# Kernel optimization log

Hardware: AMD Instinct MI355X
Metric: run time of the kernel (lower is better)

## Reference

```python
import jax, jax.numpy as jnp
import numpy as np

N, C, E = 32768, 256, 16
LN_EPS = 1e-5
ENT_EPS = 1e-12


def setup_inputs() -> dict:
    key = jax.random.key(0)
    ks = jax.random.split(key, 8)
    return {
        "inputs": jax.random.normal(ks[0], (N, C), jnp.float32),
        "conv_out": jax.random.normal(ks[1], (N, C), jnp.float32),
        "domain_emb": jax.random.normal(ks[2], (C,), jnp.float32),
        "share_W": jax.random.normal(ks[3], (C, C), jnp.float32) * 0.02,
        "share_b": jnp.zeros((C,), jnp.float32),
        "gate_W": jax.random.normal(ks[4], (C, E), jnp.float32) * 0.1,
        "gate_b": jnp.zeros((E,), jnp.float32),
        "expert_W": jax.random.normal(ks[5], (E, C, C), jnp.float32) * 0.02,
        "expert_b": jnp.zeros((E, C), jnp.float32),
        "ln_gamma": jnp.ones((C,), jnp.float32),
        "ln_beta": jnp.zeros((C,), jnp.float32),
    }


def reference(inputs, conv_out, domain_emb, share_W, share_b, gate_W, gate_b,
              expert_W, expert_b, ln_gamma, ln_beta):
    n_exp = gate_W.shape[-1]

    # shared expert
    share_out = inputs @ share_W + share_b                      # (N, C)

    # LayerNorm on (stand-in) sparse-conv features + domain embedding
    mu = conv_out.mean(-1, keepdims=True)
    var = conv_out.var(-1, keepdims=True)
    route = (conv_out - mu) / jnp.sqrt(var + LN_EPS) * ln_gamma + ln_beta
    route = route + domain_emb                                   # (N, C)

    # router (eval path: no noise)
    gate_logits = route @ gate_W + gate_b                        # (N, E)
    w = jax.nn.softmax(gate_logits.astype(jnp.float32), axis=-1).astype(inputs.dtype)

    # entropy -> dynamic k per token
    entropy = -jnp.sum(w * jnp.log(w + ENT_EPS), axis=-1)        # (N,)
    max_entropy = jnp.log(jnp.float32(n_exp))
    k = jnp.ceil(1.0 + entropy / max_entropy * (n_exp - 1)).astype(jnp.int32)
    k = jnp.clip(k, 1, n_exp)                                    # (N,)

    # dynamic top-k selection mask (sort descending, keep first k)
    order = jnp.argsort(-w, axis=-1)                             # (N, E) descending ranks
    positions = jnp.arange(n_exp)[None, :]
    mask_sorted = positions < k[:, None]                         # (N, E) bool
    inv = jnp.argsort(order, axis=-1)                            # inverse permutation
    sel_mask = jnp.take_along_axis(mask_sorted, inv, axis=-1)    # (N, E) bool, expert-order
    combine = jnp.where(sel_mask, w, jnp.zeros_like(w))          # (N, E) combine weights

    # Switch-style load balancing loss
    frac_tokens = sel_mask.astype(jnp.float32).mean(0)           # (E,)
    frac_probs = w.astype(jnp.float32).mean(0)                   # (E,)
    loss_balance = jnp.mean(frac_tokens * frac_probs) * (n_exp ** 2)

    # expert compute + combine (dense, equivalent to gather/scatter loop)
    expert_out = jnp.einsum('nc,ecd->ned', inputs, expert_W) + expert_b  # (N, E, C)
    moe_out = jnp.einsum('ne,nec->nc', combine, expert_out)     # (N, C)

    return moe_out + share_out, loss_balance
```

## Files before the change

kernel.cpp:

```cpp
#include <hip/hip_runtime.h>
#include <hip/hip_bf16.h>

#define NTOK 32768
#define CH   256
#define NEXP 16

typedef __attribute__((ext_vector_type(8)))  short short8;
typedef __attribute__((ext_vector_type(16))) float f32x16;

#define MFMA32(a, b, c) __builtin_amdgcn_mfma_f32_32x32x16_bf16((a), (b), (c), 0, 0, 0)
#define BC8(v) __builtin_bit_cast(short8, (v))

#define GLD16(lds, g) __builtin_amdgcn_global_load_lds(                          \
    (const __attribute__((address_space(1))) unsigned int*)(g),                  \
    (__attribute__((address_space(3))) unsigned int*)(lds), 16, 0, 0)

static __device__ __forceinline__ unsigned short f2bf(float f) {
  unsigned int u = __builtin_bit_cast(unsigned int, f);
  unsigned int r = (u + 0x7fffu + ((u >> 16) & 1u)) >> 16;
  return (unsigned short)r;
}


__global__ __launch_bounds__(256) void wconvert_kernel(
    const float* __restrict__ share_W, const float* __restrict__ expert_W,
    uint4* __restrict__ wp) {
  int g = blockIdx.x * 256 + threadIdx.x;
  int e = g >> 13;
  int r = g & 8191;
  int lane = r & 63;
  int kb = (r >> 6) & 15;
  int db = r >> 10;
  int d  = db * 32 + (lane & 31);
  int k0 = kb * 16 + ((lane >> 5) << 3);
  const float* src = (e < 16) ? (expert_W + (size_t)e * 65536) : share_W;
  unsigned int p[4];
#pragma unroll
  for (int j = 0; j < 4; j++) {
    float f0 = src[(size_t)(k0 + 2 * j) * 256 + d];
    float f1 = src[(size_t)(k0 + 2 * j + 1) * 256 + d];
    p[j] = (unsigned int)f2bf(f0) | ((unsigned int)f2bf(f1) << 16);
  }
  wp[g] = make_uint4(p[0], p[1], p[2], p[3]);
}

__global__ __launch_bounds__(512, 2) void gate_kernel(
    const float* __restrict__ inputs, const float* __restrict__ conv_out,
    const float* __restrict__ domain_emb, const float* __restrict__ gate_W,
    const float* __restrict__ gate_b, const float* __restrict__ ln_gamma,
    const float* __restrict__ ln_beta, uint4* __restrict__ apack,
    float* __restrict__ combine, float* __restrict__ frac_part) {
  __shared__ __align__(16) unsigned short atile[64 * 256];
  __shared__ __align__(16) float gwT[16 * 260];
  __shared__ float route[8][256];
  __shared__ float fred[2][8][16];
  int t = threadIdx.x, b = blockIdx.x;
  int w = t >> 6, l = t & 63;

  for (int i = 0; i < 8; i++) {
    int idx = i * 512 + t;
    gwT[(idx & 15) * 260 + (idx >> 4)] = gate_W[idx];
  }

  for (int i = 0; i < 4; i++) {
    int idx = i * 512 + t;
    int row = idx >> 5;
    int j = idx & 31;
    const float4* src = (const float4*)(inputs + ((size_t)b * 64 + row) * 256 + j * 8);
    float4 f0 = src[0], f1 = src[1];
    unsigned int p0 = (unsigned int)f2bf(f0.x) | ((unsigned int)f2bf(f0.y) << 16);
    unsigned int p1 = (unsigned int)f2bf(f0.z) | ((unsigned int)f2bf(f0.w) << 16);
    unsigned int p2 = (unsigned int)f2bf(f1.x) | ((unsigned int)f2bf(f1.y) << 16);
    unsigned int p3 = (unsigned int)f2bf(f1.z) | ((unsigned int)f2bf(f1.w) << 16);
    int s = j ^ (row & 31);
    *(uint4*)(atile + (row * 32 + s) * 8) = make_uint4(p0, p1, p2, p3);
  }
  __syncthreads();
  for (int i = 0; i < 4; i++) {
    int L = i * 512 + t;
    int ll = L & 63;
    int mb = (L >> 6) & 1, kb = L >> 7;
    int row = mb * 32 + (ll & 31);
    int j = kb * 2 + (ll >> 5);
    int s = j ^ (row & 31);
    apack[(size_t)b * 2048 + L] = *(const uint4*)(atile + (row * 32 + s) * 8);
  }

  int lc = l * 4;
  float4 g4 = *(const float4*)(ln_gamma + lc);
  float4 be4 = *(const float4*)(ln_beta + lc);
  float4 de4 = *(const float4*)(domain_emb + lc);
  int e = l & 15, q = l >> 4;
  float gb = gate_b[e];
  float psel = 0.f, pw = 0.f;

  float4 gwreg[16];
#pragma unroll
  for (int ii = 0; ii < 16; ii++)
    gwreg[ii] = *(const float4*)&gwT[e * 260 + q * 64 + ii * 4];

  int n0 = b * 64 + w * 8;
  float4 x = *(const float4*)(conv_out + (size_t)n0 * 256 + lc);
  for (int i = 0; i < 8; i++) {
    float4 xn = *(const float4*)(conv_out + (size_t)(n0 + ((i + 1) & 7)) * 256 + lc);

    float s1 = x.x + x.y + x.z + x.w;
#pragma unroll
    for (int off = 1; off < 64; off <<= 1) s1 += __shfl_xor(s1, off);
    float mu = s1 * (1.f / 256.f);
    float dx = x.x - mu, dy = x.y - mu, dz = x.z - mu, dw = x.w - mu;
    float s2 = dx * dx + dy * dy + dz * dz + dw * dw;
#pragma unroll
    for (int off = 1; off < 64; off <<= 1) s2 += __shfl_xor(s2, off);
    float rstd = rsqrtf(s2 * (1.f / 256.f) + 1e-5f);
    float4 r;
    r.x = dx * rstd * g4.x + be4.x + de4.x;
    r.y = dy * rstd * g4.y + be4.y + de4.y;
    r.z = dz * rstd * g4.z + be4.z + de4.z;
    r.w = dw * rstd * g4.w + be4.w + de4.w;
    *(float4*)(&route[w][lc]) = r;
    asm volatile("s_waitcnt lgkmcnt(0)" ::: "memory");
    __builtin_amdgcn_wave_barrier();

    float a0 = 0.f, a1 = 0.f, a2 = 0.f, a3 = 0.f;
#pragma unroll
    for (int ii = 0; ii < 16; ii += 4) {
      float4 r0 = *(const float4*)(&route[w][q * 64 + (ii + 0) * 4]);
      float4 r1 = *(const float4*)(&route[w][q * 64 + (ii + 1) * 4]);
      float4 r2 = *(const float4*)(&route[w][q * 64 + (ii + 2) * 4]);
      float4 r3 = *(const float4*)(&route[w][q * 64 + (ii + 3) * 4]);
      a0 += r0.x * gwreg[ii + 0].x + r0.y * gwreg[ii + 0].y + r0.z * gwreg[ii + 0].z + r0.w * gwreg[ii + 0].w;
      a1 += r1.x * gwreg[ii + 1].x + r1.y * gwreg[ii + 1].y + r1.z * gwreg[ii + 1].z + r1.w * gwreg[ii + 1].w;
      a2 += r2.x * gwreg[ii + 2].x + r2.y * gwreg[ii + 2].y + r2.z * gwreg[ii + 2].z + r2.w * gwreg[ii + 2].w;
      a3 += r3.x * gwreg[ii + 3].x + r3.y * gwreg[ii + 3].y + r3.z * gwreg[ii + 3].z + r3.w * gwreg[ii + 3].w;
    }
    float acc = (a0 + a1) + (a2 + a3);
    acc += __shfl_xor(acc, 16);
    acc += __shfl_xor(acc, 32);
    float logit = acc + gb;

    float m = logit;
#pragma unroll
    for (int off = 1; off < 16; off <<= 1) m = fmaxf(m, __shfl_xor(m, off));
    float p = expf(logit - m);
    float sum = p;
#pragma unroll
    for (int off = 1; off < 16; off <<= 1) sum += __shfl_xor(sum, off);
    float wv = p / sum;

    float et = -wv * logf(wv + 1e-12f);
    float ent = et;
#pragma unroll
    for (int off = 1; off < 16; off <<= 1) ent += __shfl_xor(ent, off);
    float kf = ceilf(1.f + ent * (15.f / 2.7725887f));
    int k = (int)kf;
    k = max(1, min(16, k));

    int base = l & 48;
    int rank = 0;
#pragma unroll
    for (int j = 0; j < 16; j++) {
      float wj = __shfl(wv, base + j);
      rank += (wj > wv) || (wj == wv && j < e);
    }
    int sel = rank < k;
    float cmb = sel ? wv : 0.f;
    int n = n0 + i;
    if (l < 16) combine[(size_t)n * 16 + e] = cmb;
    psel += (float)sel;
    pw += wv;

    x = xn;
  }

  if (l < 16) { fred[0][w][l] = psel; fred[1][w][l] = pw; }
  __syncthreads();
  if (t < 32) {
    int kind = t >> 4, ee = t & 15;
    float v = 0.f;
#pragma unroll
    for (int ww = 0; ww < 8; ww++) v += fred[kind][ww][ee];
    frac_part[b * 32 + t] = v;
  }
}

static __device__ __forceinline__ void pref_b(
    uint4 (&breg)[8], const uint4* __restrict__ we, int q) {
#pragma unroll
  for (int f = 0; f < 8; f++) {
    int kbl = f >> 1, d = f & 1;
    breg[f] = we[(size_t)d * 1024 + (q * 4 + kbl) * 64];
  }
}

static __device__ __forceinline__ void slot_mfma(
    f32x16 (&tacc)[2][2], const f32x16& zc, const uint4* __restrict__ ab,
    const uint4 (&breg)[8], int q, bool first) {
  __builtin_amdgcn_s_setprio(1);
#pragma unroll
  for (int kbl = 0; kbl < 4; kbl++) {
    short8 a0 = BC8(ab[(q * 4 + kbl) * 256]);
    short8 a1 = BC8(ab[(q * 4 + kbl) * 256 + 64]);
    short8 b0 = BC8(breg[kbl * 2 + 0]);
    short8 b1 = BC8(breg[kbl * 2 + 1]);
    if (first && kbl == 0) {
      tacc[0][0] = MFMA32(a0, b0, zc);
      tacc[0][1] = MFMA32(a0, b1, zc);
      tacc[1][0] = MFMA32(a1, b0, zc);
      tacc[1][1] = MFMA32(a1, b1, zc);
    } else {
      tacc[0][0] = MFMA32(a0, b0, tacc[0][0]);
      tacc[0][1] = MFMA32(a0, b1, tacc[0][1]);
      tacc[1][0] = MFMA32(a1, b0, tacc[1][0]);
      tacc[1][1] = MFMA32(a1, b1, tacc[1][1]);
    }
  }
  __builtin_amdgcn_s_setprio(0);
}

__global__ __launch_bounds__(512, 2) void moe_gemm_kernel(
    const uint4* __restrict__ apack, const uint4* __restrict__ wpack,
    const float* __restrict__ combine, const float* __restrict__ expert_b,
    const float* __restrict__ share_b, float* __restrict__ out) {
  extern __shared__ __align__(16) char smem[];
  uint4* atile = (uint4*)smem;
  float* wtile = (float*)(smem + 65536);

  int t = threadIdx.x, b = blockIdx.x;
  int w = t >> 6, l = t & 63;
  int mbp = w >> 2;
  int dbp = w & 3;

#pragma unroll
  for (int i = 0; i < 8; i++) {
    int g = w * 8 + i;
    int kb = g >> 2, mb = g & 3;
    const uint4* src = apack + ((size_t)(2 * b + (mb >> 1)) * 2048 + (size_t)(kb * 2 + (mb & 1)) * 64 + l);
    GLD16(atile + g * 64, src);
  }
  {
    const float* cg = combine + (size_t)b * 2048;
#pragma unroll
    for (int i = 0; i < 4; i++) {
      int idx = i * 512 + t;
      wtile[(idx & 15) * 128 + (idx >> 4)] = cg[idx];
    }
  }
  __syncthreads();

  f32x16 facc[2][2];
#pragma unroll
  for (int mi = 0; mi < 2; mi++)
#pragma unroll
    for (int d = 0; d < 2; d++)
#pragma unroll
      for (int r = 0; r < 16; r++) facc[mi][d][r] = 0.f;
  f32x16 zc;
#pragma unroll
  for (int r = 0; r < 16; r++) zc[r] = 0.f;

  f32x16 tacc[2][2];
  int rowoff = (l >> 5) * 4;

  const uint4* ab = atile + (size_t)(mbp * 2) * 64 + l;
  const uint4* wb = wpack + (size_t)(dbp * 2) * 1024 + l;

  uint4 bregA[8], bregB[8];
  pref_b(bregA, wb, 0);

  for (int e = 0; e < 17; e++) {
    const uint4* we = wb + (size_t)e * 8192;
    pref_b(bregB, we, 1);
    slot_mfma(tacc, zc, ab, bregA, 0, true);
    pref_b(bregA, we, 2);
    slot_mfma(tacc, zc, ab, bregB, 1, false);
    pref_b(bregB, we, 3);
    slot_mfma(tacc, zc, ab, bregA, 2, false);
    if (e < 16) pref_b(bregA, we + 8192, 0);
    slot_mfma(tacc, zc, ab, bregB, 3, false);

    if (e < 16) {
#pragma unroll
      for (int mi = 0; mi < 2; mi++)
#pragma unroll
        for (int rg = 0; rg < 4; rg++) {
          float4 w4 = *(const float4*)&wtile[e * 128 + (mbp * 2 + mi) * 32 + 8 * rg + rowoff];
          float wj[4] = {w4.x, w4.y, w4.z, w4.w};
#pragma unroll
          for (int j = 0; j < 4; j++) {
            facc[mi][0][rg * 4 + j] += wj[j] * tacc[mi][0][rg * 4 + j];
            facc[mi][1][rg * 4 + j] += wj[j] * tacc[mi][1][rg * 4 + j];
          }
        }
    } else {
#pragma unroll
      for (int mi = 0; mi < 2; mi++)
#pragma unroll
        for (int r = 0; r < 16; r++) {
          facc[mi][0][r] += tacc[mi][0][r];
          facc[mi][1][r] += tacc[mi][1][r];
        }
    }
  }

  int col = l & 31;
  int cg0 = (dbp * 2 + 0) * 32 + col;
  int cg1 = (dbp * 2 + 1) * 32 + col;
  float sb0 = share_b[cg0], sb1 = share_b[cg1];
  float eb0[16], eb1[16];
#pragma unroll
  for (int e2 = 0; e2 < 16; e2++) {
    eb0[e2] = expert_b[e2 * 256 + cg0];
    eb1[e2] = expert_b[e2 * 256 + cg1];
  }
#pragma unroll
  for (int e2 = 0; e2 < 16; e2++)
#pragma unroll
    for (int mi = 0; mi < 2; mi++)
#pragma unroll
      for (int rg = 0; rg < 4; rg++) {
        float4 w4 = *(const float4*)&wtile[e2 * 128 + (mbp * 2 + mi) * 32 + 8 * rg + rowoff];
        float wj[4] = {w4.x, w4.y, w4.z, w4.w};
#pragma unroll
        for (int j = 0; j < 4; j++) {
          facc[mi][0][rg * 4 + j] += wj[j] * eb0[e2];
          facc[mi][1][rg * 4 + j] += wj[j] * eb1[e2];
        }
      }
#pragma unroll
  for (int mi = 0; mi < 2; mi++)
#pragma unroll
    for (int r = 0; r < 16; r++) {
      int row = (mbp * 2 + mi) * 32 + (r & 3) + ((r >> 2) << 3) + rowoff;
      size_t n = (size_t)b * 128 + row;
      out[n * 256 + cg0] = facc[mi][0][r] + sb0;
      out[n * 256 + cg1] = facc[mi][1][r] + sb1;
    }
}

__global__ __launch_bounds__(256) void finalize_kernel(
    const float* __restrict__ frac_part, float* __restrict__ loss_out) {
  __shared__ float acc[8][32];
  int t = threadIdx.x;
  int col = t & 31, seg = t >> 5;
  float s = 0.f;
  for (int i = seg; i < 512; i += 8) s += frac_part[i * 32 + col];
  acc[seg][col] = s;
  __syncthreads();
  if (t < 32) {
    float v = 0.f;
#pragma unroll
    for (int sg = 0; sg < 8; sg++) v += acc[sg][t];
    acc[0][t] = v;
  }
  __syncthreads();
  if (t == 0) {
    float loss = 0.f;
    for (int e = 0; e < 16; e++) {
      float ft = acc[0][e] * (1.f / 32768.f);
      float fp = acc[0][16 + e] * (1.f / 32768.f);
      loss += ft * fp;
    }
    loss_out[0] = loss * 16.f;
  }
}

extern "C" void kernel_launch(void* const* d_in, const int* in_sizes, int n_in,
                              void* d_out, int out_size, void* d_ws, size_t ws_size,
                              hipStream_t stream) {
  const float* inputs   = (const float*)d_in[0];
  const float* conv_out = (const float*)d_in[1];
  const float* demb     = (const float*)d_in[2];
  const float* share_W  = (const float*)d_in[3];
  const float* share_b  = (const float*)d_in[4];
  const float* gate_W   = (const float*)d_in[5];
  const float* gate_b   = (const float*)d_in[6];
  const float* expert_W = (const float*)d_in[7];
  const float* expert_b = (const float*)d_in[8];
  const float* ln_g     = (const float*)d_in[9];
  const float* ln_b     = (const float*)d_in[10];
  float* out = (float*)d_out;
  char* ws = (char*)d_ws;

  uint4* apack   = (uint4*)(ws);
  uint4* wpack   = (uint4*)(ws + 16777216);
  float* combine = (float*)(ws + 19005440);
  float* frac    = (float*)(ws + 21102592);

  hipFuncSetAttribute((const void*)moe_gemm_kernel,
                      hipFuncAttributeMaxDynamicSharedMemorySize, 73728);

  wconvert_kernel<<<dim3(544), dim3(256), 0, stream>>>(share_W, expert_W, wpack);
  gate_kernel<<<dim3(512), dim3(512), 0, stream>>>(inputs, conv_out, demb, gate_W,
                                                   gate_b, ln_g, ln_b, apack, combine, frac);
  moe_gemm_kernel<<<dim3(256), dim3(512), 73728, stream>>>(apack, wpack, combine,
                                                           expert_b, share_b, out);
  finalize_kernel<<<dim3(1), dim3(256), 0, stream>>>(frac, out + 8388608);
}
```

Before: 241.0 us.

## Fuse gating and expert GEMM into one kernel, removing apack/combine round trips

Merges the gate kernel (LayerNorm, router, softmax, entropy-based top-k) with the MoE GEMM kernel so the bf16 input tile and the combine weights stay in LDS instead of going through global workspace. The gate weight transpose moves into an extra block of the weight-convert kernel. The GEMM tile shrinks to 64 rows per block with one 32-column block per wave, and occupancy rises to 4 blocks. Each block now re-streams all expert weights for half as many rows, which doubles weight traffic from L2, and MFMA reuse per weight load drops.

```diff
diff --git a/kernel.cpp b/kernel.cpp
--- a/kernel.cpp
+++ b/kernel.cpp
@@ -10,10 +10,6 @@
 
 #define MFMA32(a, b, c) __builtin_amdgcn_mfma_f32_32x32x16_bf16((a), (b), (c), 0, 0, 0)
 #define BC8(v) __builtin_bit_cast(short8, (v))
-
-#define GLD16(lds, g) __builtin_amdgcn_global_load_lds(                          \
-    (const __attribute__((address_space(1))) unsigned int*)(g),                  \
-    (__attribute__((address_space(3))) unsigned int*)(lds), 16, 0, 0)
 
 static __device__ __forceinline__ unsigned short f2bf(float f) {
   unsigned int u = __builtin_bit_cast(unsigned int, f);
@@ -24,7 +20,17 @@
 
 __global__ __launch_bounds__(256) void wconvert_kernel(
     const float* __restrict__ share_W, const float* __restrict__ expert_W,
-    uint4* __restrict__ wp) {
+    const float* __restrict__ gate_W, uint4* __restrict__ wp,
+    float* __restrict__ gwt) {
+  if (blockIdx.x == 544) {
+    int t = threadIdx.x;
+#pragma unroll
+    for (int i = 0; i < 16; i++) {
+      int idx = i * 256 + t;
+      gwt[(idx & 15) * 256 + (idx >> 4)] = gate_W[idx];
+    }
+    return;
+  }
   int g = blockIdx.x * 256 + threadIdx.x;
   int e = g >> 13;
   int r = g & 8191;
@@ -44,297 +50,232 @@
   wp[g] = make_uint4(p[0], p[1], p[2], p[3]);
 }
 
-__global__ __launch_bounds__(512, 2) void gate_kernel(
+static __device__ __forceinline__ void slot_mfma4(
+    f32x16 (&tacc)[2], const f32x16& zc, const uint4* __restrict__ at,
+    const uint4 (&breg)[4], int q, int r5, int hi, bool first) {
+  __builtin_amdgcn_s_setprio(1);
+#pragma unroll
+  for (int kbl = 0; kbl < 4; kbl++) {
+    int kb = q * 4 + kbl;
+    int ai = r5 * 32 + ((kb * 2 + hi) ^ r5);
+    short8 a0 = BC8(at[ai]);
+    short8 a1 = BC8(at[1024 + ai]);
+    short8 bb = BC8(breg[kbl]);
+    if (first && kbl == 0) {
+      tacc[0] = MFMA32(a0, bb, zc);
+      tacc[1] = MFMA32(a1, bb, zc);
+    } else {
+      tacc[0] = MFMA32(a0, bb, tacc[0]);
+      tacc[1] = MFMA32(a1, bb, tacc[1]);
+    }
+  }
+  __builtin_amdgcn_s_setprio(0);
+}
+
+__global__ __launch_bounds__(512, 4) void moe_fused_kernel(
     const float* __restrict__ inputs, const float* __restrict__ conv_out,
-    const float* __restrict__ domain_emb, const float* __restrict__ gate_W,
+    const float* __restrict__ domain_emb, const float* __restrict__ gwt,
     const float* __restrict__ gate_b, const float* __restrict__ ln_gamma,
-    const float* __restrict__ ln_beta, uint4* __restrict__ apack,
-    float* __restrict__ combine, float* __restrict__ frac_part) {
-  __shared__ __align__(16) unsigned short atile[64 * 256];
-  __shared__ __align__(16) float gwT[16 * 260];
-  __shared__ float route[8][256];
-  __shared__ float fred[2][8][16];
+    const float* __restrict__ ln_beta, const uint4* __restrict__ wpack,
+    const float* __restrict__ expert_b, const float* __restrict__ share_b,
+    float* __restrict__ out, float* __restrict__ frac_part) {
+  extern __shared__ __align__(16) char smem[];
+  uint4* at    = (uint4*)smem;
+  float* wtile = (float*)(smem + 32768);
+  float* route = (float*)(smem + 36864);
+
   int t = threadIdx.x, b = blockIdx.x;
   int w = t >> 6, l = t & 63;
-
-  for (int i = 0; i < 8; i++) {
-    int idx = i * 512 + t;
-    gwT[(idx & 15) * 260 + (idx >> 4)] = gate_W[idx];
-  }
-
+  int dbp = w;
+  int r5 = l & 31, hi = l >> 5;
+
+#pragma unroll
   for (int i = 0; i < 4; i++) {
     int idx = i * 512 + t;
-    int row = idx >> 5;
-    int j = idx & 31;
-    const float4* src = (const float4*)(inputs + ((size_t)b * 64 + row) * 256 + j * 8);
+    int r = idx >> 5, j = idx & 31;
+    const float4* src = (const float4*)(inputs + ((size_t)b * 64 + r) * 256 + j * 8);
     float4 f0 = src[0], f1 = src[1];
     unsigned int p0 = (unsigned int)f2bf(f0.x) | ((unsigned int)f2bf(f0.y) << 16);
     unsigned int p1 = (unsigned int)f2bf(f0.z) | ((unsigned int)f2bf(f0.w) << 16);
     unsigned int p2 = (unsigned int)f2bf(f1.x) | ((unsigned int)f2bf(f1.y) << 16);
     unsigned int p3 = (unsigned int)f2bf(f1.z) | ((unsigned int)f2bf(f1.w) << 16);
-    int s = j ^ (row & 31);
-    *(uint4*)(atile + (row * 32 + s) * 8) = make_uint4(p0, p1, p2, p3);
-  }
-  __syncthreads();
-  for (int i = 0; i < 4; i++) {
-    int L = i * 512 + t;
-    int ll = L & 63;
-    int mb = (L >> 6) & 1, kb = L >> 7;
-    int row = mb * 32 + (ll & 31);
-    int j = kb * 2 + (ll >> 5);
-    int s = j ^ (row & 31);
-    apack[(size_t)b * 2048 + L] = *(const uint4*)(atile + (row * 32 + s) * 8);
-  }
-
-  int lc = l * 4;
-  float4 g4 = *(const float4*)(ln_gamma + lc);
-  float4 be4 = *(const float4*)(ln_beta + lc);
-  float4 de4 = *(const float4*)(domain_emb + lc);
-  int e = l & 15, q = l >> 4;
-  float gb = gate_b[e];
-  float psel = 0.f, pw = 0.f;
-
-  float4 gwreg[16];
-#pragma unroll
-  for (int ii = 0; ii < 16; ii++)
-    gwreg[ii] = *(const float4*)&gwT[e * 260 + q * 64 + ii * 4];
-
-  int n0 = b * 64 + w * 8;
-  float4 x = *(const float4*)(conv_out + (size_t)n0 * 256 + lc);
-  for (int i = 0; i < 8; i++) {
-    float4 xn = *(const float4*)(conv_out + (size_t)(n0 + ((i + 1) & 7)) * 256 + lc);
-
-    float s1 = x.x + x.y + x.z + x.w;
-#pragma unroll
-    for (int off = 1; off < 64; off <<= 1) s1 += __shfl_xor(s1, off);
-    float mu = s1 * (1.f / 256.f);
-    float dx = x.x - mu, dy = x.y - mu, dz = x.z - mu, dw = x.w - mu;
-    float s2 = dx * dx + dy * dy + dz * dz + dw * dw;
-#pragma unroll
-    for (int off = 1; off < 64; off <<= 1) s2 += __shfl_xor(s2, off);
-    float rstd = rsqrtf(s2 * (1.f / 256.f) + 1e-5f);
-    float4 r;
-    r.x = dx * rstd * g4.x + be4.x + de4.x;
-    r.y = dy * rstd * g4.y + be4.y + de4.y;
-    r.z = dz * rstd * g4.z + be4.z + de4.z;
-    r.w = dw * rstd * g4.w + be4.w + de4.w;
-    *(float4*)(&route[w][lc]) = r;
-    asm volatile("s_waitcnt lgkmcnt(0)" ::: "memory");
-    __builtin_amdgcn_wave_barrier();
-
-    float a0 = 0.f, a1 = 0.f, a2 = 0.f, a3 = 0.f;
-#pragma unroll
-    for (int ii = 0; ii < 16; ii += 4) {
-      float4 r0 = *(const float4*)(&route[w][q * 64 + (ii + 0) * 4]);
-      float4 r1 = *(const float4*)(&route[w][q * 64 + (ii + 1) * 4]);
-      float4 r2 = *(const float4*)(&route[w][q * 64 + (ii + 2) * 4]);
-      float4 r3 = *(const float4*)(&route[w][q * 64 + (ii + 3) * 4]);
-      a0 += r0.x * gwreg[ii + 0].x + r0.y * gwreg[ii + 0].y + r0.z * gwreg[ii + 0].z + r0.w * gwreg[ii + 0].w;
-      a1 += r1.x * gwreg[ii + 1].x + r1.y * gwreg[ii + 1].y + r1.z * gwreg[ii + 1].z + r1.w * gwreg[ii + 1].w;
-      a2 += r2.x * gwreg[ii + 2].x + r2.y * gwreg[ii + 2].y + r2.z * gwreg[ii + 2].z + r2.w * gwreg[ii + 2].w;
-      a3 += r3.x * gwreg[ii + 3].x + r3.y * gwreg[ii + 3].y + r3.z * gwreg[ii + 3].z + r3.w * gwreg[ii + 3].w;
-    }
-    float acc = (a0 + a1) + (a2 + a3);
-    acc += __shfl_xor(acc, 16);
-    acc += __shfl_xor(acc, 32);
-    float logit = acc + gb;
-
-    float m = logit;
-#pragma unroll
-    for (int off = 1; off < 16; off <<= 1) m = fmaxf(m, __shfl_xor(m, off));
-    float p = expf(logit - m);
-    float sum = p;
-#pragma unroll
-    for (int off = 1; off < 16; off <<= 1) sum += __shfl_xor(sum, off);
-    float wv = p / sum;
-
-    float et = -wv * logf(wv + 1e-12f);
-    float ent = et;
-#pragma unroll
-    for (int off = 1; off < 16; off <<= 1) ent += __shfl_xor(ent, off);
-    float kf = ceilf(1.f + ent * (15.f / 2.7725887f));
-    int k = (int)kf;
-    k = max(1, min(16, k));
-
-    int base = l & 48;
-    int rank = 0;
-#pragma unroll
-    for (int j = 0; j < 16; j++) {
-      float wj = __shfl(wv, base + j);
-      rank += (wj > wv) || (wj == wv && j < e);
-    }
-    int sel = rank < k;
-    float cmb = sel ? wv : 0.f;
-    int n = n0 + i;
-    if (l < 16) combine[(size_t)n * 16 + e] = cmb;
-    psel += (float)sel;
-    pw += wv;
-
-    x = xn;
-  }
-
-  if (l < 16) { fred[0][w][l] = psel; fred[1][w][l] = pw; }
-  __syncthreads();
-  if (t < 32) {
-    int kind = t >> 4, ee = t & 15;
-    float v = 0.f;
-#pragma unroll
-    for (int ww = 0; ww < 8; ww++) v += fred[kind][ww][ee];
-    frac_part[b * 32 + t] = v;
-  }
-}
-
-static __device__ __forceinline__ void pref_b(
-    uint4 (&breg)[8], const uint4* __restrict__ we, int q) {
-#pragma unroll
-  for (int f = 0; f < 8; f++) {
-    int kbl = f >> 1, d = f & 1;
-    breg[f] = we[(size_t)d * 1024 + (q * 4 + kbl) * 64];
-  }
-}
-
-static __device__ __forceinline__ void slot_mfma(
-    f32x16 (&tacc)[2][2], const f32x16& zc, const uint4* __restrict__ ab,
-    const uint4 (&breg)[8], int q, bool first) {
-  __builtin_amdgcn_s_setprio(1);
-#pragma unroll
-  for (int kbl = 0; kbl < 4; kbl++) {
-    short8 a0 = BC8(ab[(q * 4 + kbl) * 256]);
-    short8 a1 = BC8(ab[(q * 4 + kbl) * 256 + 64]);
-    short8 b0 = BC8(breg[kbl * 2 + 0]);
-    short8 b1 = BC8(breg[kbl * 2 + 1]);
-    if (first && kbl == 0) {
-      tacc[0][0] = MFMA32(a0, b0, zc);
-      tacc[0][1] = MFMA32(a0, b1, zc);
-      tacc[1][0] = MFMA32(a1, b0, zc);
-      tacc[1][1] = MFMA32(a1, b1, zc);
-    } else {
-      tacc[0][0] = MFMA32(a0, b0, tacc[0][0]);
-      tacc[0][1] = MFMA32(a0, b1, tacc[0][1]);
-      tacc[1][0] = MFMA32(a1, b0, tacc[1][0]);
-      tacc[1][1] = MFMA32(a1, b1, tacc[1][1]);
-    }
-  }
-  __builtin_amdgcn_s_setprio(0);
-}
-
-__global__ __launch_bounds__(512, 2) void moe_gemm_kernel(
-    const uint4* __restrict__ apack, const uint4* __restrict__ wpack,
-    const float* __restrict__ combine, const float* __restrict__ expert_b,
-    const float* __restrict__ share_b, float* __restrict__ out) {
-  extern __shared__ __align__(16) char smem[];
-  uint4* atile = (uint4*)smem;
-  float* wtile = (float*)(smem + 65536);
-
-  int t = threadIdx.x, b = blockIdx.x;
-  int w = t >> 6, l = t & 63;
-  int mbp = w >> 2;
-  int dbp = w & 3;
-
-#pragma unroll
-  for (int i = 0; i < 8; i++) {
-    int g = w * 8 + i;
-    int kb = g >> 2, mb = g & 3;
-    const uint4* src = apack + ((size_t)(2 * b + (mb >> 1)) * 2048 + (size_t)(kb * 2 + (mb & 1)) * 64 + l);
-    GLD16(atile + g * 64, src);
-  }
+    at[r * 32 + (j ^ (r & 31))] = make_uint4(p0, p1, p2, p3);
+  }
+
+  const uint4* wb = wpack + (size_t)dbp * 1024 + l;
+  uint4 bregA[4], bregB[4];
+#pragma unroll
+  for (int kbl = 0; kbl < 4; kbl++) bregA[kbl] = wb[kbl * 64];
+
   {
-    const float* cg = combine + (size_t)b * 2048;
-#pragma unroll
-    for (int i = 0; i < 4; i++) {
-      int idx = i * 512 + t;
-      wtile[(idx & 15) * 128 + (idx >> 4)] = cg[idx];
-    }
-  }
-  __syncthreads();
-
-  f32x16 facc[2][2];
+    int lc = l * 4;
+    float4 g4 = *(const float4*)(ln_gamma + lc);
+    float4 be4 = *(const float4*)(ln_beta + lc);
+    float4 de4 = *(const float4*)(domain_emb + lc);
+    int e = l & 15, q = l >> 4;
+    float gb = gate_b[e];
+    const float4* gv4 = (const float4*)(gwt + e * 256 + q * 64);
+    float psel = 0.f, pw = 0.f;
+
+    int n0 = b * 64 + w * 8;
+    float4 x = *(const float4*)(conv_out + (size_t)n0 * 256 + lc);
+    for (int i = 0; i < 8; i++) {
+      float4 xn = *(const float4*)(conv_out + (size_t)(n0 + ((i + 1) & 7)) * 256 + lc);
+
+      float s1 = x.x + x.y + x.z + x.w;
+#pragma unroll
+      for (int off = 1; off < 64; off <<= 1) s1 += __shfl_xor(s1, off);
+      float mu = s1 * (1.f / 256.f);
+      float dx = x.x - mu, dy = x.y - mu, dz = x.z - mu, dw = x.w - mu;
+      float s2 = dx * dx + dy * dy + dz * dz + dw * dw;
+#pragma unroll
+      for (int off = 1; off < 64; off <<= 1) s2 += __shfl_xor(s2, off);
+      float rstd = rsqrtf(s2 * (1.f / 256.f) + 1e-5f);
+      float4 r;
+      r.x = dx * rstd * g4.x + be4.x + de4.x;
+      r.y = dy * rstd * g4.y + be4.y + de4.y;
+      r.z = dz * rstd * g4.z + be4.z + de4.z;
+      r.w = dw * rstd * g4.w + be4.w + de4.w;
+      *(float4*)(&route[w * 256 + lc]) = r;
+      asm volatile("s_waitcnt lgkmcnt(0)" ::: "memory");
+      __builtin_amdgcn_wave_barrier();
+
+      float a0 = 0.f, a1 = 0.f, a2 = 0.f, a3 = 0.f;
+#pragma unroll
+      for (int ii = 0; ii < 16; ii += 4) {
+        float4 r0 = *(const float4*)(&route[w * 256 + q * 64 + (ii + 0) * 4]);
+        float4 r1 = *(const float4*)(&route[w * 256 + q * 64 + (ii + 1) * 4]);
+        float4 r2 = *(const float4*)(&route[w * 256 + q * 64 + (ii + 2) * 4]);
+        float4 r3 = *(const float4*)(&route[w * 256 + q * 64 + (ii + 3) * 4]);
+        float4 g0 = gv4[ii + 0], g1 = gv4[ii + 1], g2 = gv4[ii + 2], g3 = gv4[ii + 3];
+        a0 += r0.x * g0.x + r0.y * g0.y + r0.z * g0.z + r0.w * g0.w;
+        a1 += r1.x * g1.x + r1.y * g1.y + r1.z * g1.z + r1.w * g1.w;
+        a2 += r2.x * g2.x + r2.y * g2.y + r2.z * g2.z + r2.w * g2.w;
+        a3 += r3.x * g3.x + r3.y * g3.y + r3.z * g3.z + r3.w * g3.w;
+      }
+      float acc = (a0 + a1) + (a2 + a3);
+      acc += __shfl_xor(acc, 16);
+      acc += __shfl_xor(acc, 32);
+      float logit = acc + gb;
+
+      float m = logit;
+#pragma unroll
+      for (int off = 1; off < 16; off <<= 1) m = fmaxf(m, __shfl_xor(m, off));
+      float p = expf(logit - m);
+      float sum = p;
+#pragma unroll
+      for (int off = 1; off < 16; off <<= 1) sum += __shfl_xor(sum, off);
+      float wv = p / sum;
+
+      float et = -wv * logf(wv + 1e-12f);
+      float ent = et;
+#pragma unroll
+      for (int off = 1; off < 16; off <<= 1) ent += __shfl_xor(ent, off);
+      float kf = ceilf(1.f + ent * (15.f / 2.7725887f));
+      int k = (int)kf;
+      k = max(1, min(16, k));
+
+      int base = l & 48;
+      int rank = 0;
+#pragma unroll
+      for (int j = 0; j < 16; j++) {
+        float wj = __shfl(wv, base + j);
+        rank += (wj > wv) || (wj == wv && j < e);
+      }
+      int sel = rank < k;
+      float cmb = sel ? wv : 0.f;
+      if (l < 16) wtile[e * 64 + (w * 8 + i)] = cmb;
+      psel += (float)sel;
+      pw += wv;
+
+      x = xn;
+    }
+
+    __syncthreads();
+    if (l < 16) {
+      route[0 * 128 + w * 16 + l] = psel;
+      route[1 * 128 + w * 16 + l] = pw;
+    }
+    __syncthreads();
+    if (t < 32) {
+      int kind = t >> 4, ee = t & 15;
+      float v = 0.f;
+#pragma unroll
+      for (int ww = 0; ww < 8; ww++) v += route[kind * 128 + ww * 16 + ee];
+      frac_part[b * 32 + t] = v;
+    }
+  }
+
+  f32x16 facc[2];
 #pragma unroll
   for (int mi = 0; mi < 2; mi++)
 #pragma unroll
-    for (int d = 0; d < 2; d++)
-#pragma unroll
-      for (int r = 0; r < 16; r++) facc[mi][d][r] = 0.f;
+    for (int r = 0; r < 16; r++) facc[mi][r] = 0.f;
   f32x16 zc;
 #pragma unroll
   for (int r = 0; r < 16; r++) zc[r] = 0.f;
-
-  f32x16 tacc[2][2];
-  int rowoff = (l >> 5) * 4;
-
-  const uint4* ab = atile + (size_t)(mbp * 2) * 64 + l;
-  const uint4* wb = wpack + (size_t)(dbp * 2) * 1024 + l;
-
-  uint4 bregA[8], bregB[8];
-  pref_b(bregA, wb, 0);
+  f32x16 tacc[2];
+  int rowoff = hi * 4;
 
   for (int e = 0; e < 17; e++) {
     const uint4* we = wb + (size_t)e * 8192;
-    pref_b(bregB, we, 1);
-    slot_mfma(tacc, zc, ab, bregA, 0, true);
-    pref_b(bregA, we, 2);
-    slot_mfma(tacc, zc, ab, bregB, 1, false);
-    pref_b(bregB, we, 3);
-    slot_mfma(tacc, zc, ab, bregA, 2, false);
-    if (e < 16) pref_b(bregA, we + 8192, 0);
-    slot_mfma(tacc, zc, ab, bregB, 3, false);
-
+#pragma unroll
+    for (int kbl = 0; kbl < 4; kbl++) bregB[kbl] = we[(4 + kbl) * 64];
+    slot_mfma4(tacc, zc, at, bregA, 0, r5, hi, true);
+#pragma unroll
+    for (int kbl = 0; kbl < 4; kbl++) bregA[kbl] = we[(8 + kbl) * 64];
+    slot_mfma4(tacc, zc, at, bregB, 1, r5, hi, false);
+#pragma unroll
+    for (int kbl = 0; kbl < 4; kbl++) bregB[kbl] = we[(12 + kbl) * 64];
+    slot_mfma4(tacc, zc, at, bregA, 2, r5, hi, false);
     if (e < 16) {
 #pragma unroll
+      for (int kbl = 0; kbl < 4; kbl++) bregA[kbl] = we[8192 + kbl * 64];
+    }
+    slot_mfma4(tacc, zc, at, bregB, 3, r5, hi, false);
+
+    if (e < 16) {
+#pragma unroll
       for (int mi = 0; mi < 2; mi++)
 #pragma unroll
         for (int rg = 0; rg < 4; rg++) {
-          float4 w4 = *(const float4*)&wtile[e * 128 + (mbp * 2 + mi) * 32 + 8 * rg + rowoff];
+          float4 w4 = *(const float4*)&wtile[e * 64 + mi * 32 + 8 * rg + rowoff];
           float wj[4] = {w4.x, w4.y, w4.z, w4.w};
 #pragma unroll
-          for (int j = 0; j < 4; j++) {
-            facc[mi][0][rg * 4 + j] += wj[j] * tacc[mi][0][rg * 4 + j];
-            facc[mi][1][rg * 4 + j] += wj[j] * tacc[mi][1][rg * 4 + j];
-          }
+          for (int j = 0; j < 4; j++)
+            facc[mi][rg * 4 + j] += wj[j] * tacc[mi][rg * 4 + j];
         }
     } else {
 #pragma unroll
       for (int mi = 0; mi < 2; mi++)
 #pragma unroll
-        for (int r = 0; r < 16; r++) {
-          facc[mi][0][r] += tacc[mi][0][r];
-          facc[mi][1][r] += tacc[mi][1][r];
-        }
-    }
-  }
-
-  int col = l & 31;
-  int cg0 = (dbp * 2 + 0) * 32 + col;
-  int cg1 = (dbp * 2 + 1) * 32 + col;
-  float sb0 = share_b[cg0], sb1 = share_b[cg1];
-  float eb0[16], eb1[16];
-#pragma unroll
-  for (int e2 = 0; e2 < 16; e2++) {
-    eb0[e2] = expert_b[e2 * 256 + cg0];
-    eb1[e2] = expert_b[e2 * 256 + cg1];
-  }
+        for (int r = 0; r < 16; r++) facc[mi][r] += tacc[mi][r];
+    }
+  }
+
+  int col = dbp * 32 + r5;
+  float sb = share_b[col];
+  float eb[16];
+#pragma unroll
+  for (int e2 = 0; e2 < 16; e2++) eb[e2] = expert_b[e2 * 256 + col];
 #pragma unroll
   for (int e2 = 0; e2 < 16; e2++)
 #pragma unroll
     for (int mi = 0; mi < 2; mi++)
 #pragma unroll
       for (int rg = 0; rg < 4; rg++) {
-        float4 w4 = *(const float4*)&wtile[e2 * 128 + (mbp * 2 + mi) * 32 + 8 * rg + rowoff];
+        float4 w4 = *(const float4*)&wtile[e2 * 64 + mi * 32 + 8 * rg + rowoff];
         float wj[4] = {w4.x, w4.y, w4.z, w4.w};
 #pragma unroll
-        for (int j = 0; j < 4; j++) {
-          facc[mi][0][rg * 4 + j] += wj[j] * eb0[e2];
-          facc[mi][1][rg * 4 + j] += wj[j] * eb1[e2];
-        }
+        for (int j = 0; j < 4; j++)
+          facc[mi][rg * 4 + j] += wj[j] * eb[e2];
       }
 #pragma unroll
   for (int mi = 0; mi < 2; mi++)
 #pragma unroll
     for (int r = 0; r < 16; r++) {
-      int row = (mbp * 2 + mi) * 32 + (r & 3) + ((r >> 2) << 3) + rowoff;
-      size_t n = (size_t)b * 128 + row;
-      out[n * 256 + cg0] = facc[mi][0][r] + sb0;
-      out[n * 256 + cg1] = facc[mi][1][r] + sb1;
+      int row = mi * 32 + (r & 3) + ((r >> 2) << 3) + rowoff;
+      out[((size_t)b * 64 + row) * 256 + col] = facc[mi][r] + sb;
     }
 }
 
@@ -382,18 +323,17 @@
   float* out = (float*)d_out;
   char* ws = (char*)d_ws;
 
-  uint4* apack   = (uint4*)(ws);
-  uint4* wpack   = (uint4*)(ws + 16777216);
-  float* combine = (float*)(ws + 19005440);
-  float* frac    = (float*)(ws + 21102592);
-
-  hipFuncSetAttribute((const void*)moe_gemm_kernel,
-                      hipFuncAttributeMaxDynamicSharedMemorySize, 73728);
-
-  wconvert_kernel<<<dim3(544), dim3(256), 0, stream>>>(share_W, expert_W, wpack);
-  gate_kernel<<<dim3(512), dim3(512), 0, stream>>>(inputs, conv_out, demb, gate_W,
-                                                   gate_b, ln_g, ln_b, apack, combine, frac);
-  moe_gemm_kernel<<<dim3(256), dim3(512), 73728, stream>>>(apack, wpack, combine,
-                                                           expert_b, share_b, out);
+  uint4* wpack = (uint4*)(ws);
+  float* gwt   = (float*)(ws + 2228224);
+  float* frac  = (float*)(ws + 2244608);
+
+  hipFuncSetAttribute((const void*)moe_fused_kernel,
+                      hipFuncAttributeMaxDynamicSharedMemorySize, 45056);
+
+  wconvert_kernel<<<dim3(545), dim3(256), 0, stream>>>(share_W, expert_W, gate_W,
+                                                       wpack, gwt);
+  moe_fused_kernel<<<dim3(512), dim3(512), 45056, stream>>>(
+      inputs, conv_out, demb, gwt, gate_b, ln_g, ln_b, wpack,
+      expert_b, share_b, out, frac);
   finalize_kernel<<<dim3(1), dim3(256), 0, stream>>>(frac, out + 8388608);
 }
```

Result: slower. 291.3 us (+20.9%).

## Convert inputs to bf16 inside the GEMM kernel instead of staging through apack

Applied to the files above, without the earlier changes.

The fp32 to bf16 conversion and swizzled packing of the inputs tile moves out of the gate kernel and into the MoE GEMM kernel. That kernel now loads fp32 inputs directly and writes them into LDS with an XOR swizzle, which removes the intermediate apack write and read through global memory. The gate_W transpose also moves into an extra block of the weight-convert kernel, so the gate kernel no longer stages it through LDS and its shared memory use drops. The cost is more global load bytes and conversion ALU work in the GEMM kernel's prologue, which now uses register loads instead of direct-to-LDS loads.

```diff
diff --git a/kernel.cpp b/kernel.cpp
--- a/kernel.cpp
+++ b/kernel.cpp
@@ -10,10 +10,6 @@
 
 #define MFMA32(a, b, c) __builtin_amdgcn_mfma_f32_32x32x16_bf16((a), (b), (c), 0, 0, 0)
 #define BC8(v) __builtin_bit_cast(short8, (v))
-
-#define GLD16(lds, g) __builtin_amdgcn_global_load_lds(                          \
-    (const __attribute__((address_space(1))) unsigned int*)(g),                  \
-    (__attribute__((address_space(3))) unsigned int*)(lds), 16, 0, 0)
 
 static __device__ __forceinline__ unsigned short f2bf(float f) {
   unsigned int u = __builtin_bit_cast(unsigned int, f);
@@ -24,7 +20,17 @@
 
 __global__ __launch_bounds__(256) void wconvert_kernel(
     const float* __restrict__ share_W, const float* __restrict__ expert_W,
-    uint4* __restrict__ wp) {
+    const float* __restrict__ gate_W, uint4* __restrict__ wp,
+    float* __restrict__ gwt) {
+  if (blockIdx.x == 544) {
+    int t = threadIdx.x;
+#pragma unroll
+    for (int i = 0; i < 16; i++) {
+      int idx = i * 256 + t;
+      gwt[(idx & 15) * 256 + (idx >> 4)] = gate_W[idx];
+    }
+    return;
+  }
   int g = blockIdx.x * 256 + threadIdx.x;
   int e = g >> 13;
   int r = g & 8191;
@@ -45,46 +51,14 @@
 }
 
 __global__ __launch_bounds__(512, 2) void gate_kernel(
-    const float* __restrict__ inputs, const float* __restrict__ conv_out,
-    const float* __restrict__ domain_emb, const float* __restrict__ gate_W,
-    const float* __restrict__ gate_b, const float* __restrict__ ln_gamma,
-    const float* __restrict__ ln_beta, uint4* __restrict__ apack,
+    const float* __restrict__ conv_out, const float* __restrict__ domain_emb,
+    const float* __restrict__ gwt, const float* __restrict__ gate_b,
+    const float* __restrict__ ln_gamma, const float* __restrict__ ln_beta,
     float* __restrict__ combine, float* __restrict__ frac_part) {
-  __shared__ __align__(16) unsigned short atile[64 * 256];
-  __shared__ __align__(16) float gwT[16 * 260];
   __shared__ float route[8][256];
   __shared__ float fred[2][8][16];
   int t = threadIdx.x, b = blockIdx.x;
   int w = t >> 6, l = t & 63;
-
-  for (int i = 0; i < 8; i++) {
-    int idx = i * 512 + t;
-    gwT[(idx & 15) * 260 + (idx >> 4)] = gate_W[idx];
-  }
-
-  for (int i = 0; i < 4; i++) {
-    int idx = i * 512 + t;
-    int row = idx >> 5;
-    int j = idx & 31;
-    const float4* src = (const float4*)(inputs + ((size_t)b * 64 + row) * 256 + j * 8);
-    float4 f0 = src[0], f1 = src[1];
-    unsigned int p0 = (unsigned int)f2bf(f0.x) | ((unsigned int)f2bf(f0.y) << 16);
-    unsigned int p1 = (unsigned int)f2bf(f0.z) | ((unsigned int)f2bf(f0.w) << 16);
-    unsigned int p2 = (unsigned int)f2bf(f1.x) | ((unsigned int)f2bf(f1.y) << 16);
-    unsigned int p3 = (unsigned int)f2bf(f1.z) | ((unsigned int)f2bf(f1.w) << 16);
-    int s = j ^ (row & 31);
-    *(uint4*)(atile + (row * 32 + s) * 8) = make_uint4(p0, p1, p2, p3);
-  }
-  __syncthreads();
-  for (int i = 0; i < 4; i++) {
-    int L = i * 512 + t;
-    int ll = L & 63;
-    int mb = (L >> 6) & 1, kb = L >> 7;
-    int row = mb * 32 + (ll & 31);
-    int j = kb * 2 + (ll >> 5);
-    int s = j ^ (row & 31);
-    apack[(size_t)b * 2048 + L] = *(const uint4*)(atile + (row * 32 + s) * 8);
-  }
 
   int lc = l * 4;
   float4 g4 = *(const float4*)(ln_gamma + lc);
@@ -92,13 +66,13 @@
   float4 de4 = *(const float4*)(domain_emb + lc);
   int e = l & 15, q = l >> 4;
   float gb = gate_b[e];
+
+  float4 gwreg[16];
+  const float4* gv4 = (const float4*)(gwt + e * 256 + q * 64);
+#pragma unroll
+  for (int ii = 0; ii < 16; ii++) gwreg[ii] = gv4[ii];
+
   float psel = 0.f, pw = 0.f;
-
-  float4 gwreg[16];
-#pragma unroll
-  for (int ii = 0; ii < 16; ii++)
-    gwreg[ii] = *(const float4*)&gwT[e * 260 + q * 64 + ii * 4];
-
   int n0 = b * 64 + w * 8;
   float4 x = *(const float4*)(conv_out + (size_t)n0 * 256 + lc);
   for (int i = 0; i < 8; i++) {
@@ -194,13 +168,15 @@
 }
 
 static __device__ __forceinline__ void slot_mfma(
-    f32x16 (&tacc)[2][2], const f32x16& zc, const uint4* __restrict__ ab,
-    const uint4 (&breg)[8], int q, bool first) {
+    f32x16 (&tacc)[2][2], const f32x16& zc, const uint4* __restrict__ at,
+    const uint4 (&breg)[8], int q, int abase, int r5, bool first) {
   __builtin_amdgcn_s_setprio(1);
 #pragma unroll
   for (int kbl = 0; kbl < 4; kbl++) {
-    short8 a0 = BC8(ab[(q * 4 + kbl) * 256]);
-    short8 a1 = BC8(ab[(q * 4 + kbl) * 256 + 64]);
+    int kb = q * 4 + kbl;
+    int ax = kb * 256 + abase + (r5 ^ kb);
+    short8 a0 = BC8(at[ax]);
+    short8 a1 = BC8(at[ax + 64]);
     short8 b0 = BC8(breg[kbl * 2 + 0]);
     short8 b1 = BC8(breg[kbl * 2 + 1]);
     if (first && kbl == 0) {
@@ -219,24 +195,33 @@
 }
 
 __global__ __launch_bounds__(512, 2) void moe_gemm_kernel(
-    const uint4* __restrict__ apack, const uint4* __restrict__ wpack,
+    const float* __restrict__ inputs, const uint4* __restrict__ wpack,
     const float* __restrict__ combine, const float* __restrict__ expert_b,
     const float* __restrict__ share_b, float* __restrict__ out) {
   extern __shared__ __align__(16) char smem[];
-  uint4* atile = (uint4*)smem;
+  uint4* at    = (uint4*)smem;
   float* wtile = (float*)(smem + 65536);
 
   int t = threadIdx.x, b = blockIdx.x;
   int w = t >> 6, l = t & 63;
   int mbp = w >> 2;
   int dbp = w & 3;
+  int r5 = l & 31, hi = l >> 5;
 
 #pragma unroll
   for (int i = 0; i < 8; i++) {
-    int g = w * 8 + i;
-    int kb = g >> 2, mb = g & 3;
-    const uint4* src = apack + ((size_t)(2 * b + (mb >> 1)) * 2048 + (size_t)(kb * 2 + (mb & 1)) * 64 + l);
-    GLD16(atile + g * 64, src);
+    int idx = i * 512 + t;
+    int row = idx >> 5;
+    int j = idx & 31;
+    const float4* src = (const float4*)(inputs + ((size_t)b * 128 + row) * 256 + j * 8);
+    float4 f0 = src[0], f1 = src[1];
+    unsigned int p0 = (unsigned int)f2bf(f0.x) | ((unsigned int)f2bf(f0.y) << 16);
+    unsigned int p1 = (unsigned int)f2bf(f0.z) | ((unsigned int)f2bf(f0.w) << 16);
+    unsigned int p2 = (unsigned int)f2bf(f1.x) | ((unsigned int)f2bf(f1.y) << 16);
+    unsigned int p3 = (unsigned int)f2bf(f1.z) | ((unsigned int)f2bf(f1.w) << 16);
+    int kb = j >> 1, hib = j & 1;
+    at[kb * 256 + (row >> 5) * 64 + hib * 32 + ((row & 31) ^ kb)] =
+        make_uint4(p0, p1, p2, p3);
   }
   {
     const float* cg = combine + (size_t)b * 2048;
@@ -246,6 +231,11 @@
       wtile[(idx & 15) * 128 + (idx >> 4)] = cg[idx];
     }
   }
+
+  const uint4* wb = wpack + (size_t)(dbp * 2) * 1024 + l;
+  uint4 bregA[8], bregB[8];
+  pref_b(bregA, wb, 0);
+
   __syncthreads();
 
   f32x16 facc[2][2];
@@ -260,24 +250,19 @@
   for (int r = 0; r < 16; r++) zc[r] = 0.f;
 
   f32x16 tacc[2][2];
-  int rowoff = (l >> 5) * 4;
-
-  const uint4* ab = atile + (size_t)(mbp * 2) * 64 + l;
-  const uint4* wb = wpack + (size_t)(dbp * 2) * 1024 + l;
-
-  uint4 bregA[8], bregB[8];
-  pref_b(bregA, wb, 0);
+  int rowoff = hi * 4;
+  int abase = mbp * 128 + hi * 32;
 
   for (int e = 0; e < 17; e++) {
     const uint4* we = wb + (size_t)e * 8192;
     pref_b(bregB, we, 1);
-    slot_mfma(tacc, zc, ab, bregA, 0, true);
+    slot_mfma(tacc, zc, at, bregA, 0, abase, r5, true);
     pref_b(bregA, we, 2);
-    slot_mfma(tacc, zc, ab, bregB, 1, false);
+    slot_mfma(tacc, zc, at, bregB, 1, abase, r5, false);
     pref_b(bregB, we, 3);
-    slot_mfma(tacc, zc, ab, bregA, 2, false);
+    slot_mfma(tacc, zc, at, bregA, 2, abase, r5, false);
     if (e < 16) pref_b(bregA, we + 8192, 0);
-    slot_mfma(tacc, zc, ab, bregB, 3, false);
+    slot_mfma(tacc, zc, at, bregB, 3, abase, r5, false);
 
     if (e < 16) {
 #pragma unroll
@@ -303,7 +288,7 @@
     }
   }
 
-  int col = l & 31;
+  int col = r5;
   int cg0 = (dbp * 2 + 0) * 32 + col;
   int cg1 = (dbp * 2 + 1) * 32 + col;
   float sb0 = share_b[cg0], sb1 = share_b[cg1];
@@ -382,18 +367,19 @@
   float* out = (float*)d_out;
   char* ws = (char*)d_ws;
 
-  uint4* apack   = (uint4*)(ws);
-  uint4* wpack   = (uint4*)(ws + 16777216);
-  float* combine = (float*)(ws + 19005440);
-  float* frac    = (float*)(ws + 21102592);
+  uint4* wpack   = (uint4*)(ws);
+  float* gwt     = (float*)(ws + 2228224);
+  float* combine = (float*)(ws + 2244608);
+  float* frac    = (float*)(ws + 4341760);
 
   hipFuncSetAttribute((const void*)moe_gemm_kernel,
                       hipFuncAttributeMaxDynamicSharedMemorySize, 73728);
 
-  wconvert_kernel<<<dim3(544), dim3(256), 0, stream>>>(share_W, expert_W, wpack);
-  gate_kernel<<<dim3(512), dim3(512), 0, stream>>>(inputs, conv_out, demb, gate_W,
-                                                   gate_b, ln_g, ln_b, apack, combine, frac);
-  moe_gemm_kernel<<<dim3(256), dim3(512), 73728, stream>>>(apack, wpack, combine,
+  wconvert_kernel<<<dim3(545), dim3(256), 0, stream>>>(share_W, expert_W, gate_W,
+                                                       wpack, gwt);
+  gate_kernel<<<dim3(512), dim3(512), 0, stream>>>(conv_out, demb, gwt, gate_b,
+                                                   ln_g, ln_b, combine, frac);
+  moe_gemm_kernel<<<dim3(256), dim3(512), 73728, stream>>>(inputs, wpack, combine,
                                                            expert_b, share_b, out);
   finalize_kernel<<<dim3(1), dim3(256), 0, stream>>>(frac, out + 8388608);
 }
```

New measurement: 241.2 us. About the same (+0.1%).
